# Performance work log

Hardware: AMD Instinct MI355X
Metric: run time of the kernel (lower is better)

Reference implementation:

```python
import jax, jax.numpy as jnp
import numpy as np

B, S, D, H, TB = 8, 512, 512, 8, 64
DK = D // H
SCALE = DK ** -0.5


def setup_inputs() -> dict:
    key = jax.random.key(0)
    ks = jax.random.split(key, 9)
    return {
        "query_input": jax.random.normal(ks[0], (B, S, D), jnp.float32),
        "key_input": jax.random.normal(ks[1], (B, S, D), jnp.float32),
        "batch_temporal_mat": jax.random.uniform(ks[2], (B, S, S), jnp.float32) * 100.0,
        "Wq": jax.random.normal(ks[3], (D, D), jnp.float32) * (D ** -0.5),
        "Wk": jax.random.normal(ks[4], (D, D), jnp.float32) * (D ** -0.5),
        "Wv": jax.random.normal(ks[5], (D, D), jnp.float32) * (D ** -0.5),
        "Wp": jax.random.normal(ks[6], (D, D), jnp.float32) * (D ** -0.5),
        "Wt1": jax.random.normal(ks[7], (1, TB), jnp.float32),
        "Wt2": jax.random.normal(ks[8], (TB, 1), jnp.float32) * (TB ** -0.5),
    }


def _split_heads(x):
    # [B,S,D] -> [B,H,S,DK]
    b, s, _ = x.shape
    return x.reshape(b, s, H, DK).transpose(0, 2, 1, 3)


def reference(query_input, key_input, batch_temporal_mat, Wq, Wk, Wv, Wp, Wt1, Wt2):
    q = _split_heads(query_input @ Wq)   # [B,H,S,DK]
    k = _split_heads(key_input @ Wk)
    v = _split_heads(key_input @ Wv)

    scores = jnp.einsum("bhqd,bhkd->bhqk", q, k) * SCALE  # [B,H,S,S]

    # temporal bias: 1/log(e + t) -> Dense(TB) -> leaky_relu(0.2) -> Dense(1)
    t = 1.0 / jnp.log(jnp.e + batch_temporal_mat)          # [B,S,S]
    h = t[..., None] * Wt1[0]                              # [B,S,S,TB] (Dense from 1 dim)
    h = jnp.where(h >= 0, h, 0.2 * h)                      # leaky_relu alpha=0.2
    bias = (h @ Wt2)[..., 0]                               # [B,S,S]
    scores = scores + bias[:, None]                        # broadcast over heads

    attn = jax.nn.softmax(scores, axis=-1)
    out = jnp.einsum("bhqk,bhkd->bhqd", attn, v)           # [B,H,S,DK]
    out = out.transpose(0, 2, 1, 3).reshape(query_input.shape[0], -1, D)
    return out @ Wp
```

## Files before the change

### kernel.cpp

```cpp
#include <hip/hip_runtime.h>

#define NB 8
#define NS 512
#define ND 512
#define NH 8
#define NDK 64
#define NTB 64
#define SCALE_F 0.125f

typedef short s16x8 __attribute__((ext_vector_type(8)));
typedef float floatx4 __attribute__((ext_vector_type(4)));

__device__ __forceinline__ unsigned short bf16rn(float x) {
  unsigned u = __builtin_bit_cast(unsigned, x);
  u += 0x7FFFu + ((u >> 16) & 1u);
  return (unsigned short)(u >> 16);
}
__device__ __forceinline__ s16x8 ld8(const unsigned short* p) {
  return *reinterpret_cast<const s16x8*>(p);
}
__device__ __forceinline__ floatx4 mfma16(s16x8 a, s16x8 b, floatx4 c) {
  return __builtin_amdgcn_mfma_f32_16x16x32_bf16(a, b, c, 0, 0, 0);
}

template <int ROWS>
__device__ __forceinline__ void stage_plane(unsigned short* lds,
                                            const unsigned short* src,
                                            int src_stride, int w, int lane) {
  const int r8 = lane >> 3, ck = lane & 7;
#pragma unroll
  for (int t = 0; t < ROWS / 32; t++) {
    int row = w * (ROWS / 4) + t * 8 + r8;
    uint4 v = *reinterpret_cast<const uint4*>(src + (size_t)row * src_stride + ck * 8);
    *reinterpret_cast<uint4*>(lds + row * 64 + ((ck ^ (row & 7)) * 8)) = v;
  }
}
__device__ __forceinline__ s16x8 frag(const unsigned short* plane, int row, int chunk) {
  return *reinterpret_cast<const s16x8*>(plane + row * 64 + ((chunk ^ (row & 7)) * 8));
}


__global__ __launch_bounds__(256) void prep_kernel(
    const float* __restrict__ xq, const float* __restrict__ xk,
    const float* __restrict__ tmat, const float* __restrict__ Wq,
    const float* __restrict__ Wk, const float* __restrict__ Wv,
    const float* __restrict__ Wp, const float* __restrict__ wt1,
    const float* __restrict__ wt2, unsigned short* __restrict__ xq_bf,
    unsigned short* __restrict__ xk_bf, unsigned short* __restrict__ wT,
    unsigned short* __restrict__ biasf) {
  __shared__ float tile[64][65];
  __shared__ float w1[NTB], w2[NTB];
  const int bid = blockIdx.x;

  if (bid < 256) {
    int wi = bid >> 6;
    int t = bid & 63;
    int n0 = (t >> 3) * 64, k0 = (t & 7) * 64;
    const float* Wsrc = (wi == 0) ? Wq : (wi == 1) ? Wk : (wi == 2) ? Wv : Wp;
    unsigned short* dst = wT + (size_t)wi * ND * ND;
    int tx = threadIdx.x & 63, ty = threadIdx.x >> 6;
#pragma unroll
    for (int rr = 0; rr < 16; rr++) {
      int k = rr * 4 + ty;
      tile[k][tx] = Wsrc[(size_t)(k0 + k) * ND + n0 + tx];
    }
    __syncthreads();
#pragma unroll
    for (int rr = 0; rr < 16; rr++) {
      int n = rr * 4 + ty;
      dst[(size_t)(n0 + n) * ND + k0 + tx] = bf16rn(tile[tx][n]);
    }
  } else if (bid < 768) {
    const int per = NB * NS * ND / 4;
    for (int t = (bid - 256) * 256 + (int)threadIdx.x; t < 2 * per; t += 512 * 256) {
      const float4* src;
      unsigned short* dst;
      int i;
      if (t < per) { src = (const float4*)xq; dst = xq_bf; i = t; }
      else         { src = (const float4*)xk; dst = xk_bf; i = t - per; }
      float4 v = src[i];
      ushort4 o;
      o.x = bf16rn(v.x); o.y = bf16rn(v.y);
      o.z = bf16rn(v.z); o.w = bf16rn(v.w);
      ((ushort4*)dst)[i] = o;
    }
  } else {
    if (threadIdx.x < NTB) {
      w1[threadIdx.x] = wt1[threadIdx.x];
      w2[threadIdx.x] = wt2[threadIdx.x];
    }
    __syncthreads();
    float C = 0.f;
#pragma unroll 16
    for (int j = 0; j < NTB; j++) {
      float a = w1[j];
      C += (a >= 0.f ? a : 0.2f * a) * w2[j];
    }
    const int total = NB * NS * NS / 4;
    const float E = 2.718281828459045f;
    for (int t = (bid - 768) * 256 + (int)threadIdx.x; t < total; t += 512 * 256) {
      float4 T = ((const float4*)tmat)[t];
      ushort4 o;
      o.x = __builtin_bit_cast(unsigned short, (_Float16)(C / logf(E + T.x)));
      o.y = __builtin_bit_cast(unsigned short, (_Float16)(C / logf(E + T.y)));
      o.z = __builtin_bit_cast(unsigned short, (_Float16)(C / logf(E + T.z)));
      o.w = __builtin_bit_cast(unsigned short, (_Float16)(C / logf(E + T.w)));
      ((ushort4*)biasf)[t] = o;
    }
  }
}


__global__ __launch_bounds__(256) void gemm_qkv_kernel(
    const unsigned short* __restrict__ xq_bf, const unsigned short* __restrict__ xk_bf,
    const unsigned short* __restrict__ wT, unsigned short* __restrict__ Qd,
    unsigned short* __restrict__ Kd, unsigned short* __restrict__ Vt) {
  const int z = blockIdx.z;
  const unsigned short* Ag = (z == 0) ? xq_bf : xk_bf;
  const unsigned short* Bg = wT + (size_t)z * ND * ND;
  const int m0 = blockIdx.y * 128, n0 = blockIdx.x * 64;
  const int lane = threadIdx.x & 63, w = threadIdx.x >> 6;
  const int c = lane & 15, g = lane >> 4;
  const int wm = (w >> 1) * 64, wn = (w & 1) * 32;

  __shared__ __align__(16) unsigned short Ah[128 * 64];
  __shared__ __align__(16) unsigned short Bh[64 * 64];

  floatx4 acc[4][2];
#pragma unroll
  for (int i = 0; i < 4; i++)
#pragma unroll
    for (int j = 0; j < 2; j++) acc[i][j] = (floatx4){0.f, 0.f, 0.f, 0.f};

  for (int ks = 0; ks < ND; ks += 64) {
    __syncthreads();
    stage_plane<128>(Ah, Ag + (size_t)m0 * ND + ks, ND, w, lane);
    stage_plane<64>(Bh, Bg + (size_t)n0 * ND + ks, ND, w, lane);
    __syncthreads();
#pragma unroll
    for (int hf = 0; hf < 2; hf++) {
      s16x8 ah[4], bh[2];
#pragma unroll
      for (int i = 0; i < 4; i++) ah[i] = frag(Ah, wm + i * 16 + c, hf * 4 + g);
#pragma unroll
      for (int j = 0; j < 2; j++) bh[j] = frag(Bh, wn + j * 16 + c, hf * 4 + g);
      if (z != 2) {
#pragma unroll
        for (int i = 0; i < 4; i++)
#pragma unroll
          for (int j = 0; j < 2; j++) acc[i][j] = mfma16(ah[i], bh[j], acc[i][j]);
      } else {
#pragma unroll
        for (int i = 0; i < 4; i++)
#pragma unroll
          for (int j = 0; j < 2; j++) acc[i][j] = mfma16(bh[j], ah[i], acc[i][j]);
      }
    }
  }

  if (z != 2) {
    const float sc = (z == 0) ? SCALE_F : 1.0f;
    unsigned short* D = (z == 0) ? Qd : Kd;
#pragma unroll
    for (int i = 0; i < 4; i++)
#pragma unroll
      for (int j = 0; j < 2; j++) {
        int row0 = m0 + wm + i * 16 + g * 4;
        int col = n0 + wn + j * 16 + c;
        int h2 = col >> 6, dk = col & 63;
#pragma unroll
        for (int r = 0; r < 4; r++) {
          int rr = row0 + r;
          int bb = rr >> 9, s = rr & 511;
          D[(((size_t)bb * NH + h2) * NS + s) * NDK + dk] = bf16rn(acc[i][j][r] * sc);
        }
      }
  } else {
#pragma unroll
    for (int i = 0; i < 4; i++)
#pragma unroll
      for (int j = 0; j < 2; j++) {
        int n_base = n0 + wn + j * 16 + g * 4;
        int m = m0 + wm + i * 16 + c;
        int bb = m >> 9, s = m & 511;
#pragma unroll
        for (int r = 0; r < 4; r++) {
          int n = n_base + r;
          int h2 = n >> 6, dk = n & 63;
          Vt[(((size_t)bb * NH + h2) * NDK + dk) * NS + s] = bf16rn(acc[i][j][r]);
        }
      }
  }
}

__global__ __launch_bounds__(256) void gemm_out_kernel(
    const unsigned short* __restrict__ AO, const unsigned short* __restrict__ wT,
    float* __restrict__ out) {
  const unsigned short* Bg = wT + (size_t)3 * ND * ND;
  const int m0 = blockIdx.y * 128, n0 = blockIdx.x * 64;
  const int lane = threadIdx.x & 63, w = threadIdx.x >> 6;
  const int c = lane & 15, g = lane >> 4;
  const int wm = (w >> 1) * 64, wn = (w & 1) * 32;

  __shared__ __align__(16) unsigned short Ah[128 * 64];
  __shared__ __align__(16) unsigned short Bh[64 * 64];

  floatx4 acc[4][2];
#pragma unroll
  for (int i = 0; i < 4; i++)
#pragma unroll
    for (int j = 0; j < 2; j++) acc[i][j] = (floatx4){0.f, 0.f, 0.f, 0.f};

  for (int ks = 0; ks < ND; ks += 64) {
    __syncthreads();
    stage_plane<128>(Ah, AO + (size_t)m0 * ND + ks, ND, w, lane);
    stage_plane<64>(Bh, Bg + (size_t)n0 * ND + ks, ND, w, lane);
    __syncthreads();
#pragma unroll
    for (int hf = 0; hf < 2; hf++) {
      s16x8 ah[4], bh[2];
#pragma unroll
      for (int i = 0; i < 4; i++) ah[i] = frag(Ah, wm + i * 16 + c, hf * 4 + g);
#pragma unroll
      for (int j = 0; j < 2; j++) bh[j] = frag(Bh, wn + j * 16 + c, hf * 4 + g);
#pragma unroll
      for (int i = 0; i < 4; i++)
#pragma unroll
        for (int j = 0; j < 2; j++) acc[i][j] = mfma16(ah[i], bh[j], acc[i][j]);
    }
  }

#pragma unroll
  for (int i = 0; i < 4; i++)
#pragma unroll
    for (int j = 0; j < 2; j++) {
      int row0 = m0 + wm + i * 16 + g * 4;
      int col = n0 + wn + j * 16 + c;
#pragma unroll
      for (int r = 0; r < 4; r++)
        out[(size_t)(row0 + r) * ND + col] = acc[i][j][r];
    }
}


__global__ __launch_bounds__(256) void attn_kernel(
    const unsigned short* __restrict__ Qd, const unsigned short* __restrict__ Kd,
    const unsigned short* __restrict__ Vt, const unsigned short* __restrict__ biasf,
    unsigned short* __restrict__ AO) {
  const int id = blockIdx.x;
  const int hh = id & 7, b = (id >> 3) & 7, qt = id >> 6;
  const int lane = threadIdx.x & 63, w = threadIdx.x >> 6;
  const int c = lane & 15, g = lane >> 4;
  const size_t hoff = ((size_t)b * NH + hh) * NS * NDK;
  const unsigned short* Kb = Kd + hoff;
  const unsigned short* Vb = Vt + hoff;
  const int qbase = qt * 16;
  const _Float16* bp = (const _Float16*)biasf;

  __shared__ __align__(16) char shmem[15360];
  unsigned short* Pw = (unsigned short*)shmem + w * (16 * 72);
  float* scratch = (float*)shmem;

  s16x8 qf[2];
  {
    const unsigned short* Qb = Qd + hoff;
    size_t off = (size_t)(qbase + c) * NDK + g * 8;
    qf[0] = ld8(Qb + off);
    qf[1] = ld8(Qb + off + 32);
  }

  floatx4 acc_o[4];
#pragma unroll
  for (int d = 0; d < 4; d++) acc_o[d] = (floatx4){0.f, 0.f, 0.f, 0.f};
  float ps[4] = {0.f, 0.f, 0.f, 0.f};

#pragma unroll
  for (int kt = 0; kt < 2; kt++) {
    const int key0 = w * 128 + kt * 64;
    float bb[4][4];
#pragma unroll
    for (int f = 0; f < 4; f++)
#pragma unroll
      for (int r = 0; r < 4; r++)
        bb[f][r] = (float)bp[((size_t)b * NS + qbase + g * 4 + r) * NS + key0 + f * 16 + c];

    floatx4 sc[4];
#pragma unroll
    for (int f = 0; f < 4; f++) {
      const unsigned short* kp = Kb + (size_t)(key0 + f * 16 + c) * NDK + g * 8;
      s16x8 k0 = ld8(kp);
      s16x8 k1 = ld8(kp + 32);
      floatx4 zz = (floatx4){0.f, 0.f, 0.f, 0.f};
      zz = mfma16(qf[0], k0, zz);
      sc[f] = mfma16(qf[1], k1, zz);
    }

#pragma unroll
    for (int f = 0; f < 4; f++)
#pragma unroll
      for (int r = 0; r < 4; r++) {
        float p = __expf(sc[f][r] + bb[f][r]);
        ps[r] += p;
        Pw[(g * 4 + r) * 72 + f * 16 + c] = bf16rn(p);
      }

#pragma unroll
    for (int kf = 0; kf < 2; kf++) {
      s16x8 pf = *reinterpret_cast<const s16x8*>(&Pw[c * 72 + kf * 32 + g * 8]);
#pragma unroll
      for (int d = 0; d < 4; d++) {
        s16x8 vf = ld8(Vb + (size_t)(d * 16 + c) * NS + key0 + kf * 32 + g * 8);
        acc_o[d] = mfma16(pf, vf, acc_o[d]);
      }
    }
  }

  __syncthreads();
  if (w > 0) {
    float* s = scratch + (size_t)(w - 1) * 20 * 64;
#pragma unroll
    for (int d = 0; d < 4; d++)
#pragma unroll
      for (int r = 0; r < 4; r++) s[(d * 4 + r) * 64 + lane] = acc_o[d][r];
#pragma unroll
    for (int r = 0; r < 4; r++) s[(16 + r) * 64 + lane] = ps[r];
  }
  __syncthreads();
  if (w == 0) {
#pragma unroll
    for (int ww = 0; ww < 3; ww++) {
      const float* s = scratch + (size_t)ww * 20 * 64;
#pragma unroll
      for (int d = 0; d < 4; d++)
#pragma unroll
        for (int r = 0; r < 4; r++) acc_o[d][r] += s[(d * 4 + r) * 64 + lane];
#pragma unroll
      for (int r = 0; r < 4; r++) ps[r] += s[(16 + r) * 64 + lane];
    }
#pragma unroll
    for (int r = 0; r < 4; r++) {
#pragma unroll
      for (int mask = 1; mask < 16; mask <<= 1)
        ps[r] += __shfl_xor(ps[r], mask, 64);
    }
#pragma unroll
    for (int r = 0; r < 4; r++) {
      float inv = 1.0f / ps[r];
      int qrow = qbase + g * 4 + r;
#pragma unroll
      for (int d = 0; d < 4; d++)
        AO[((size_t)b * NS + qrow) * ND + hh * NDK + d * 16 + c] =
            bf16rn(acc_o[d][r] * inv);
    }
  }
}


extern "C" void kernel_launch(void* const* d_in, const int* in_sizes, int n_in,
                              void* d_out, int out_size, void* d_ws, size_t ws_size,
                              hipStream_t stream) {
  const float* xq = (const float*)d_in[0];
  const float* xk = (const float*)d_in[1];
  const float* tmat = (const float*)d_in[2];
  const float* Wq = (const float*)d_in[3];
  const float* Wk = (const float*)d_in[4];
  const float* Wv = (const float*)d_in[5];
  const float* Wp = (const float*)d_in[6];
  const float* Wt1 = (const float*)d_in[7];
  const float* Wt2 = (const float*)d_in[8];
  float* out = (float*)d_out;

  char* ws = (char*)d_ws;
  const size_t MB = 1u << 20;
  unsigned short* xq_bf = (unsigned short*)(ws + 0 * MB);
  unsigned short* xk_bf = (unsigned short*)(ws + 4 * MB);
  unsigned short* wT = (unsigned short*)(ws + 8 * MB);
  unsigned short* biasf = (unsigned short*)(ws + 10 * MB);
  unsigned short* Qd = (unsigned short*)(ws + 14 * MB);
  unsigned short* Kd = (unsigned short*)(ws + 18 * MB);
  unsigned short* Vt = (unsigned short*)(ws + 22 * MB);
  unsigned short* AO = (unsigned short*)(ws + 26 * MB);

  prep_kernel<<<1280, 256, 0, stream>>>(xq, xk, tmat, Wq, Wk, Wv, Wp, Wt1, Wt2,
                                        xq_bf, xk_bf, wT, biasf);
  gemm_qkv_kernel<<<dim3(8, 32, 3), 256, 0, stream>>>(xq_bf, xk_bf, wT, Qd, Kd, Vt);
  attn_kernel<<<2048, 256, 0, stream>>>(Qd, Kd, Vt, biasf, AO);
  gemm_out_kernel<<<dim3(8, 32), 256, 0, stream>>>(AO, wT, out);
}
```

Measured before the change: 146.1 us.

## Use 128x128 GEMM tiles with direct global-to-LDS loads in projection kernels

Widens the N tile of the QKV and output projection GEMMs from 64 to 128, giving each wave a 64x64 output with 16 accumulators. This halves the grid and improves operand reuse per LDS load. The register-staged tile copy is replaced by global_load_lds, which writes straight into LDS, with the swizzle applied on the global address side. The larger tile costs more registers and leaves fewer blocks (128 for the output GEMM, 384 for QKV) to fill 256 CUs.

```diff
diff --git a/kernel.cpp b/kernel.cpp
--- a/kernel.cpp
+++ b/kernel.cpp
@@ -23,21 +23,15 @@
   return __builtin_amdgcn_mfma_f32_16x16x32_bf16(a, b, c, 0, 0, 0);
 }
 
-template <int ROWS>
-__device__ __forceinline__ void stage_plane(unsigned short* lds,
-                                            const unsigned short* src,
-                                            int src_stride, int w, int lane) {
-  const int r8 = lane >> 3, ck = lane & 7;
-#pragma unroll
-  for (int t = 0; t < ROWS / 32; t++) {
-    int row = w * (ROWS / 4) + t * 8 + r8;
-    uint4 v = *reinterpret_cast<const uint4*>(src + (size_t)row * src_stride + ck * 8);
-    *reinterpret_cast<uint4*>(lds + row * 64 + ((ck ^ (row & 7)) * 8)) = v;
-  }
-}
+#define GLOAD16(g, l)                                                          \
+  __builtin_amdgcn_global_load_lds(                                            \
+      (const __attribute__((address_space(1))) unsigned int*)(g),              \
+      (__attribute__((address_space(3))) unsigned int*)(l), 16, 0, 0)
+
 __device__ __forceinline__ s16x8 frag(const unsigned short* plane, int row, int chunk) {
   return *reinterpret_cast<const s16x8*>(plane + row * 64 + ((chunk ^ (row & 7)) * 8));
 }
+
 
 
 __global__ __launch_bounds__(256) void prep_kernel(
@@ -118,42 +112,48 @@
   const int z = blockIdx.z;
   const unsigned short* Ag = (z == 0) ? xq_bf : xk_bf;
   const unsigned short* Bg = wT + (size_t)z * ND * ND;
-  const int m0 = blockIdx.y * 128, n0 = blockIdx.x * 64;
+  const int m0 = blockIdx.y * 128, n0 = blockIdx.x * 128;
   const int lane = threadIdx.x & 63, w = threadIdx.x >> 6;
   const int c = lane & 15, g = lane >> 4;
-  const int wm = (w >> 1) * 64, wn = (w & 1) * 32;
+  const int wm = (w >> 1) * 64, wn = (w & 1) * 64;
+  const int r8 = lane >> 3, ck = lane & 7;
 
   __shared__ __align__(16) unsigned short Ah[128 * 64];
-  __shared__ __align__(16) unsigned short Bh[64 * 64];
-
-  floatx4 acc[4][2];
+  __shared__ __align__(16) unsigned short Bh[128 * 64];
+
+  floatx4 acc[4][4];
 #pragma unroll
   for (int i = 0; i < 4; i++)
 #pragma unroll
-    for (int j = 0; j < 2; j++) acc[i][j] = (floatx4){0.f, 0.f, 0.f, 0.f};
+    for (int j = 0; j < 4; j++) acc[i][j] = (floatx4){0.f, 0.f, 0.f, 0.f};
 
   for (int ks = 0; ks < ND; ks += 64) {
     __syncthreads();
-    stage_plane<128>(Ah, Ag + (size_t)m0 * ND + ks, ND, w, lane);
-    stage_plane<64>(Bh, Bg + (size_t)n0 * ND + ks, ND, w, lane);
+#pragma unroll
+    for (int t = 0; t < 4; t++) {
+      int row = w * 32 + t * 8 + r8;
+      int sw = (ck ^ (row & 7)) * 8;
+      GLOAD16(Ag + (size_t)(m0 + row) * ND + ks + sw, Ah + (w * 32 + t * 8) * 64);
+      GLOAD16(Bg + (size_t)(n0 + row) * ND + ks + sw, Bh + (w * 32 + t * 8) * 64);
+    }
     __syncthreads();
 #pragma unroll
     for (int hf = 0; hf < 2; hf++) {
-      s16x8 ah[4], bh[2];
-#pragma unroll
-      for (int i = 0; i < 4; i++) ah[i] = frag(Ah, wm + i * 16 + c, hf * 4 + g);
-#pragma unroll
-      for (int j = 0; j < 2; j++) bh[j] = frag(Bh, wn + j * 16 + c, hf * 4 + g);
+      s16x8 af[4], bf[4];
+#pragma unroll
+      for (int i = 0; i < 4; i++) af[i] = frag(Ah, wm + i * 16 + c, hf * 4 + g);
+#pragma unroll
+      for (int j = 0; j < 4; j++) bf[j] = frag(Bh, wn + j * 16 + c, hf * 4 + g);
       if (z != 2) {
 #pragma unroll
         for (int i = 0; i < 4; i++)
 #pragma unroll
-          for (int j = 0; j < 2; j++) acc[i][j] = mfma16(ah[i], bh[j], acc[i][j]);
+          for (int j = 0; j < 4; j++) acc[i][j] = mfma16(af[i], bf[j], acc[i][j]);
       } else {
 #pragma unroll
         for (int i = 0; i < 4; i++)
 #pragma unroll
-          for (int j = 0; j < 2; j++) acc[i][j] = mfma16(bh[j], ah[i], acc[i][j]);
+          for (int j = 0; j < 4; j++) acc[i][j] = mfma16(bf[j], af[i], acc[i][j]);
       }
     }
   }
@@ -164,7 +164,7 @@
 #pragma unroll
     for (int i = 0; i < 4; i++)
 #pragma unroll
-      for (int j = 0; j < 2; j++) {
+      for (int j = 0; j < 4; j++) {
         int row0 = m0 + wm + i * 16 + g * 4;
         int col = n0 + wn + j * 16 + c;
         int h2 = col >> 6, dk = col & 63;
@@ -179,7 +179,7 @@
 #pragma unroll
     for (int i = 0; i < 4; i++)
 #pragma unroll
-      for (int j = 0; j < 2; j++) {
+      for (int j = 0; j < 4; j++) {
         int n_base = n0 + wn + j * 16 + g * 4;
         int m = m0 + wm + i * 16 + c;
         int bb = m >> 9, s = m & 511;
@@ -197,43 +197,49 @@
     const unsigned short* __restrict__ AO, const unsigned short* __restrict__ wT,
     float* __restrict__ out) {
   const unsigned short* Bg = wT + (size_t)3 * ND * ND;
-  const int m0 = blockIdx.y * 128, n0 = blockIdx.x * 64;
+  const int m0 = blockIdx.y * 128, n0 = blockIdx.x * 128;
   const int lane = threadIdx.x & 63, w = threadIdx.x >> 6;
   const int c = lane & 15, g = lane >> 4;
-  const int wm = (w >> 1) * 64, wn = (w & 1) * 32;
+  const int wm = (w >> 1) * 64, wn = (w & 1) * 64;
+  const int r8 = lane >> 3, ck = lane & 7;
 
   __shared__ __align__(16) unsigned short Ah[128 * 64];
-  __shared__ __align__(16) unsigned short Bh[64 * 64];
-
-  floatx4 acc[4][2];
+  __shared__ __align__(16) unsigned short Bh[128 * 64];
+
+  floatx4 acc[4][4];
 #pragma unroll
   for (int i = 0; i < 4; i++)
 #pragma unroll
-    for (int j = 0; j < 2; j++) acc[i][j] = (floatx4){0.f, 0.f, 0.f, 0.f};
+    for (int j = 0; j < 4; j++) acc[i][j] = (floatx4){0.f, 0.f, 0.f, 0.f};
 
   for (int ks = 0; ks < ND; ks += 64) {
     __syncthreads();
-    stage_plane<128>(Ah, AO + (size_t)m0 * ND + ks, ND, w, lane);
-    stage_plane<64>(Bh, Bg + (size_t)n0 * ND + ks, ND, w, lane);
+#pragma unroll
+    for (int t = 0; t < 4; t++) {
+      int row = w * 32 + t * 8 + r8;
+      int sw = (ck ^ (row & 7)) * 8;
+      GLOAD16(AO + (size_t)(m0 + row) * ND + ks + sw, Ah + (w * 32 + t * 8) * 64);
+      GLOAD16(Bg + (size_t)(n0 + row) * ND + ks + sw, Bh + (w * 32 + t * 8) * 64);
+    }
     __syncthreads();
 #pragma unroll
     for (int hf = 0; hf < 2; hf++) {
-      s16x8 ah[4], bh[2];
-#pragma unroll
-      for (int i = 0; i < 4; i++) ah[i] = frag(Ah, wm + i * 16 + c, hf * 4 + g);
-#pragma unroll
-      for (int j = 0; j < 2; j++) bh[j] = frag(Bh, wn + j * 16 + c, hf * 4 + g);
+      s16x8 af[4], bf[4];
+#pragma unroll
+      for (int i = 0; i < 4; i++) af[i] = frag(Ah, wm + i * 16 + c, hf * 4 + g);
+#pragma unroll
+      for (int j = 0; j < 4; j++) bf[j] = frag(Bh, wn + j * 16 + c, hf * 4 + g);
 #pragma unroll
       for (int i = 0; i < 4; i++)
 #pragma unroll
-        for (int j = 0; j < 2; j++) acc[i][j] = mfma16(ah[i], bh[j], acc[i][j]);
+        for (int j = 0; j < 4; j++) acc[i][j] = mfma16(af[i], bf[j], acc[i][j]);
     }
   }
 
 #pragma unroll
   for (int i = 0; i < 4; i++)
 #pragma unroll
-    for (int j = 0; j < 2; j++) {
+    for (int j = 0; j < 4; j++) {
       int row0 = m0 + wm + i * 16 + g * 4;
       int col = n0 + wn + j * 16 + c;
 #pragma unroll
@@ -383,7 +389,7 @@
 
   prep_kernel<<<1280, 256, 0, stream>>>(xq, xk, tmat, Wq, Wk, Wv, Wp, Wt1, Wt2,
                                         xq_bf, xk_bf, wT, biasf);
-  gemm_qkv_kernel<<<dim3(8, 32, 3), 256, 0, stream>>>(xq_bf, xk_bf, wT, Qd, Kd, Vt);
+  gemm_qkv_kernel<<<dim3(4, 32, 3), 256, 0, stream>>>(xq_bf, xk_bf, wT, Qd, Kd, Vt);
   attn_kernel<<<2048, 256, 0, stream>>>(Qd, Kd, Vt, biasf, AO);
-  gemm_out_kernel<<<dim3(8, 32), 256, 0, stream>>>(AO, wT, out);
-}
+  gemm_out_kernel<<<dim3(4, 32), 256, 0, stream>>>(AO, wT, out);
+}
```

Result: no change. 147.8 us (+1.2%).
